# Kernel tuning notes

Hardware: AMD Instinct MI355X
Metric: run time of the kernel (lower is better)

Reference implementation:

```python
import jax, jax.numpy as jnp
import numpy as np

B, N, C = 1, 384, 64
H = 1  # num_heads

def setup_inputs() -> dict:
    key = jax.random.key(0)
    k1, k2 = jax.random.split(key)
    x = jax.random.normal(k1, (B, N, C), dtype=jnp.float32)
    # Linear(dim, 8*dim, bias=False) weight, torch layout [out, in]; scaled for sane logits
    w_w = jax.random.normal(k2, (8 * C, C), dtype=jnp.float32) * 0.05
    return {"x": x, "w_w": w_w}

def reference(x, w_w):
    Bx, Nx, Cx = x.shape
    D = Cx // H
    scale = D ** (-0.5)
    # [B,N,8C] -> [8,B,H,N,D]
    w = (x @ w_w.T).reshape(Bx, Nx, 8, H, D).transpose(2, 0, 3, 1, 4)
    a, b, c, d, e, f, v1, v2 = (w[i] for i in range(8))
    AB = jnp.einsum('bhid,bhjd->bhij', a, b) * scale  # scores over (i,j)
    CD = jnp.einsum('bhid,bhkd->bhik', c, d) * scale  # scores over (i,k)
    EF = jnp.einsum('bhjd,bhkd->bhjk', e, f) * scale  # scores over (j,k)
    # A_IJK[b,h,i,j,k] = AB[i,j] + CD[i,k] + EF[j,k]
    A = AB[:, :, :, :, None] + CD[:, :, :, None, :] + EF[:, :, None, :, :]
    # original subtracts the GLOBAL max of the whole tensor
    eA = jnp.exp(A - jnp.max(A))
    # V[b,h,j,k,d] = v1[j,d] * v2[k,d]
    V = v1[:, :, :, None, :] * v2[:, :, None, :, :]
    num = jnp.einsum('bhijk,bhjkd->bhid', eA, V)  # sum over j,k (avoids N^3*D blowup)
    den = jnp.sum(eA, axis=(-2, -1))[..., None]   # [B,H,N,1]
    out = num / den
    # [B,H,N,D] -> [B,N,C]  (forward returns before self.proj)
    return jnp.transpose(out, (0, 2, 1, 3)).reshape(Bx, Nx, Cx)
```

## Files before the change

kernel.cpp:

```cpp
#include <hip/hip_runtime.h>
#include <math.h>


#define NN 384

using short8 = __attribute__((ext_vector_type(8))) short;
using f32x4  = __attribute__((ext_vector_type(4))) float;
typedef unsigned short u16;
typedef unsigned int u32;

__global__ void proj_kernel(const float* __restrict__ x, const float* __restrict__ W,
                            float* __restrict__ proj, float* __restrict__ v1t,
                            float* __restrict__ v2t) {
    int n = blockIdx.x;
    __shared__ float xs[64];
    if (threadIdx.x < 64) xs[threadIdx.x] = x[n * 64 + threadIdx.x];
    __syncthreads();
    const float4* xv4 = (const float4*)xs;
    for (int r = 0; r < 2; ++r) {
        int o = threadIdx.x + r * 256;
        const float4* w4 = (const float4*)(W + o * 64);
        float s = 0.f;
#pragma unroll
        for (int c = 0; c < 16; ++c) {
            float4 wv = w4[c];
            float4 xv = xv4[c];
            s += wv.x * xv.x + wv.y * xv.y + wv.z * xv.z + wv.w * xv.w;
        }
        proj[n * 512 + o] = s;
        if (o >= 448)      v2t[(o - 448) * NN + n] = s;
        else if (o >= 384) v1t[(o - 384) * NN + n] = s;
    }
}

__global__ void scores_exp_kernel(const float* __restrict__ proj,
                                  float* __restrict__ R, float* __restrict__ P,
                                  u16* __restrict__ Qhi, u16* __restrict__ Qlo) {
    int m = blockIdx.z;
    int bi = blockIdx.y, bj = blockIdx.x;
    int tid = threadIdx.x;
    int tx = tid % 16, ty = tid / 16;
    int aoff, boff;
    if (m == 0)      { aoff = 0;   boff = 64;  }
    else if (m == 1) { aoff = 128; boff = 192; }
    else             { aoff = 256; boff = 320; }

    __shared__ float As[32][65], Bs[32][65];
    for (int r = 0; r < 8; ++r) {
        int idx = tid + r * 256;
        int row = idx / 64, col = idx % 64;
        As[row][col] = proj[(bi * 32 + row) * 512 + aoff + col];
        Bs[row][col] = proj[(bj * 32 + row) * 512 + boff + col];
    }
    __syncthreads();

    float acc[2][2] = {{0.f, 0.f}, {0.f, 0.f}};
#pragma unroll 8
    for (int d = 0; d < 64; ++d) {
        float a0 = As[ty * 2][d], a1 = As[ty * 2 + 1][d];
        float b0 = Bs[tx * 2][d], b1 = Bs[tx * 2 + 1][d];
        acc[0][0] += a0 * b0; acc[0][1] += a0 * b1;
        acc[1][0] += a1 * b0; acc[1][1] += a1 * b1;
    }
#pragma unroll
    for (int a = 0; a < 2; ++a) {
        int row = bi * 32 + ty * 2 + a;
        int col = bj * 32 + tx * 2;
        float v0 = expf(acc[a][0] * 0.125f);
        float v1 = expf(acc[a][1] * 0.125f);
        if (m == 0) {
            R[row * NN + col] = v0; R[row * NN + col + 1] = v1;
        } else if (m == 1) {
            P[row * NN + col] = v0; P[row * NN + col + 1] = v1;
        } else {
            u32 b0 = __float_as_uint(v0), b1 = __float_as_uint(v1);
            u32 h0 = b0 & 0xFFFF0000u,   h1 = b1 & 0xFFFF0000u;
            float l0 = v0 - __uint_as_float(h0);
            float l1 = v1 - __uint_as_float(h1);
            ushort2 hw, lw;
            hw.x = (u16)(h0 >> 16); hw.y = (u16)(h1 >> 16);
            lw.x = (u16)(__float_as_uint(l0) >> 16);
            lw.y = (u16)(__float_as_uint(l1) >> 16);
            *(ushort2*)(Qhi + row * NN + col) = hw;
            *(ushort2*)(Qlo + row * NN + col) = lw;
        }
    }
}

#define MFMA(A, B, C) __builtin_amdgcn_mfma_f32_16x16x32_bf16(A, B, C, 0, 0, 0)

__global__ __launch_bounds__(256, 3) void main_mfma(
    const u16* __restrict__ Qhi, const u16* __restrict__ Qlo,
    const float* __restrict__ R, const float* __restrict__ P,
    const float* __restrict__ v1t, const float* __restrict__ v2t,
    float* __restrict__ num0, float* __restrict__ num1,
    float* __restrict__ den0, float* __restrict__ den1) {
    int i  = blockIdx.x >> 1;
    int jh = blockIdx.x & 1;
    int tid = (int)threadIdx.x;
    int w = tid >> 6, l = tid & 63;
    int lr = l & 15, lc = l >> 4;
    int j0 = jh * 192 + w * 48;

    __shared__ float p_s[NN];
    __shared__ u16 Bh[2][80 * 40];
    __shared__ u16 Bl[2][80 * 40];
    __shared__ float sh[4][80];

    p_s[tid] = P[i * NN + tid];
    if (tid < 128) p_s[256 + tid] = P[i * NN + 256 + tid];

    f32x4 acc[3][5];
#pragma unroll
    for (int mf = 0; mf < 3; ++mf)
#pragma unroll
        for (int nf = 0; nf < 5; ++nf)
            acc[mf][nf] = (f32x4){0.f, 0.f, 0.f, 0.f};

    __syncthreads();

    auto BUILD = [&](int buf, int k0) {
        {
            int n = tid >> 2, kk = (tid & 3) * 8;
            const float* vp = v2t + n * NN + k0 + kk;
            float4 va = *(const float4*)vp;
            float4 vb = *(const float4*)(vp + 4);
            float pr[8] = {va.x * p_s[k0 + kk + 0], va.y * p_s[k0 + kk + 1],
                           va.z * p_s[k0 + kk + 2], va.w * p_s[k0 + kk + 3],
                           vb.x * p_s[k0 + kk + 4], vb.y * p_s[k0 + kk + 5],
                           vb.z * p_s[k0 + kk + 6], vb.w * p_s[k0 + kk + 7]};
            u32* dh = (u32*)&Bh[buf][n * 40 + kk];
            u32* dl = (u32*)&Bl[buf][n * 40 + kk];
#pragma unroll
            for (int e = 0; e < 4; ++e) {
                float x0 = pr[2 * e], x1 = pr[2 * e + 1];
                u32 h0 = __float_as_uint(x0) & 0xFFFF0000u;
                u32 h1 = __float_as_uint(x1) & 0xFFFF0000u;
                float l0 = x0 - __uint_as_float(h0);
                float l1 = x1 - __uint_as_float(h1);
                dh[e] = (h0 >> 16) | h1;
                dl[e] = (__float_as_uint(l0) >> 16) |
                        (__float_as_uint(l1) & 0xFFFF0000u);
            }
        }
        if (tid < 64) {
            int n = 64 + (tid >> 2), kk = (tid & 3) * 8;
            u32* dh = (u32*)&Bh[buf][n * 40 + kk];
            u32* dl = (u32*)&Bl[buf][n * 40 + kk];
            if (n == 64) {
#pragma unroll
                for (int e = 0; e < 4; ++e) {
                    float x0 = p_s[k0 + kk + 2 * e], x1 = p_s[k0 + kk + 2 * e + 1];
                    u32 h0 = __float_as_uint(x0) & 0xFFFF0000u;
                    u32 h1 = __float_as_uint(x1) & 0xFFFF0000u;
                    float l0 = x0 - __uint_as_float(h0);
                    float l1 = x1 - __uint_as_float(h1);
                    dh[e] = (h0 >> 16) | h1;
                    dl[e] = (__float_as_uint(l0) >> 16) |
                            (__float_as_uint(l1) & 0xFFFF0000u);
                }
            } else {
#pragma unroll
                for (int e = 0; e < 4; ++e) { dh[e] = 0u; dl[e] = 0u; }
            }
        }
    };

    BUILD(0, 0);
    __syncthreads();

    for (int t = 0; t < 12; ++t) {
        int b = t & 1;
        int k8 = t * 32 + lc * 8;
        short8 ahi[3], alo[3];
#pragma unroll
        for (int mf = 0; mf < 3; ++mf) {
            int j = j0 + mf * 16 + lr;
            ahi[mf] = *(const short8*)(Qhi + j * NN + k8);
            alo[mf] = *(const short8*)(Qlo + j * NN + k8);
        }
        if (t < 11) BUILD(b ^ 1, (t + 1) * 32);
#pragma unroll
        for (int nf = 0; nf < 5; ++nf) {
            short8 bh = *(const short8*)&Bh[b][(nf * 16 + lr) * 40 + lc * 8];
            short8 bl = *(const short8*)&Bl[b][(nf * 16 + lr) * 40 + lc * 8];
#pragma unroll
            for (int mf = 0; mf < 3; ++mf) {
                acc[mf][nf] = MFMA(ahi[mf], bh, acc[mf][nf]);
                acc[mf][nf] = MFMA(ahi[mf], bl, acc[mf][nf]);
                acc[mf][nf] = MFMA(alo[mf], bh, acc[mf][nf]);
            }
        }
        __syncthreads();
    }

    float4 rj[3];
#pragma unroll
    for (int mf = 0; mf < 3; ++mf)
        rj[mf] = *(const float4*)(R + i * NN + j0 + mf * 16 + lc * 4);

#pragma unroll
    for (int nf = 0; nf < 5; ++nf) {
        float s = 0.f;
#pragma unroll
        for (int mf = 0; mf < 3; ++mf) {
            f32x4 a = acc[mf][nf];
            if (nf < 4) {
                const float* vp = v1t + (nf * 16 + lr) * NN + j0 + mf * 16 + lc * 4;
                float4 v1v = *(const float4*)vp;
                s += a[0] * rj[mf].x * v1v.x + a[1] * rj[mf].y * v1v.y
                   + a[2] * rj[mf].z * v1v.z + a[3] * rj[mf].w * v1v.w;
            } else {
                s += a[0] * rj[mf].x + a[1] * rj[mf].y
                   + a[2] * rj[mf].z + a[3] * rj[mf].w;
            }
        }
        s += __shfl_xor(s, 16, 64);
        s += __shfl_xor(s, 32, 64);
        if (l < 16) sh[w][nf * 16 + l] = s;
    }
    __syncthreads();
    if (tid < 80) {
        float v = sh[0][tid] + sh[1][tid] + sh[2][tid] + sh[3][tid];
        if (tid < 64) (jh ? num1 : num0)[i * 64 + tid] = v;
        else if (tid == 64) (jh ? den1 : den0)[i] = v;
    }
}

__global__ void finalize_kernel(const float* __restrict__ num0, const float* __restrict__ num1,
                                const float* __restrict__ den0, const float* __restrict__ den1,
                                float* __restrict__ out) {
    int idx = blockIdx.x * 256 + threadIdx.x;
    int i = idx >> 6;
    out[idx] = (num0[idx] + num1[idx]) / (den0[i] + den1[i]);
}

extern "C" void kernel_launch(void* const* d_in, const int* in_sizes, int n_in,
                              void* d_out, int out_size, void* d_ws, size_t ws_size,
                              hipStream_t stream) {
    const float* x = (const float*)d_in[0];
    const float* W = (const float*)d_in[1];
    float* out = (float*)d_out;

    float* ws   = (float*)d_ws;
    float* R    = ws;
    float* P    = ws + 147456;
    float* v1t  = ws + 294912;
    float* v2t  = ws + 319488;
    u16*   Qhi  = (u16*)(ws + 344064);
    u16*   Qlo  = (u16*)(ws + 417792);
    float* proj = ws + 491520;
    float* num0 = proj;
    float* num1 = proj + 24576;
    float* den0 = proj + 49152;
    float* den1 = proj + 49536;

    proj_kernel<<<NN, 256, 0, stream>>>(x, W, proj, v1t, v2t);
    scores_exp_kernel<<<dim3(12, 12, 3), 256, 0, stream>>>(proj, R, P, Qhi, Qlo);
    main_mfma<<<768, 256, 0, stream>>>(Qhi, Qlo, R, P, v1t, v2t,
                                       num0, num1, den0, den1);
    finalize_kernel<<<96, 256, 0, stream>>>(num0, num1, den0, den1, out);
}
```

Measured before the change: 105.9 us.

## Split k reduction across two blocks and reduce four partials in finalize

The main MFMA kernel now splits the k dimension in half, so 1536 blocks each run 6 k-steps instead of 768 blocks running 12. Each block writes its partial numerator and denominator to one of four slots, and the finalize kernel sums them. Zero-padding rows are cleared once at kernel start instead of inside every build step, the k loop is fully unrolled, and the launch-bounds occupancy hint rises from 3 to 4. This aims to fill more CUs and shorten the serial k loop, at the cost of extra partial writes and more register pressure from the higher occupancy target.

```diff
diff --git a/kernel.cpp b/kernel.cpp
--- a/kernel.cpp
+++ b/kernel.cpp
@@ -89,26 +89,32 @@
 
 #define MFMA(A, B, C) __builtin_amdgcn_mfma_f32_16x16x32_bf16(A, B, C, 0, 0, 0)
 
-__global__ __launch_bounds__(256, 3) void main_mfma(
+__global__ __launch_bounds__(256, 4) void main_mfma(
     const u16* __restrict__ Qhi, const u16* __restrict__ Qlo,
     const float* __restrict__ R, const float* __restrict__ P,
     const float* __restrict__ v1t, const float* __restrict__ v2t,
-    float* __restrict__ num0, float* __restrict__ num1,
-    float* __restrict__ den0, float* __restrict__ den1) {
-    int i  = blockIdx.x >> 1;
-    int jh = blockIdx.x & 1;
+    float* __restrict__ numP, float* __restrict__ denP) {
+    int bid = blockIdx.x;
+    int i  = bid >> 2;
+    int jh = (bid >> 1) & 1;
+    int kh = bid & 1;
     int tid = (int)threadIdx.x;
     int w = tid >> 6, l = tid & 63;
     int lr = l & 15, lc = l >> 4;
     int j0 = jh * 192 + w * 48;
-
-    __shared__ float p_s[NN];
+    int kbase = kh * 192;
+
+    __shared__ float p_s[192];
     __shared__ u16 Bh[2][80 * 40];
     __shared__ u16 Bl[2][80 * 40];
     __shared__ float sh[4][80];
 
-    p_s[tid] = P[i * NN + tid];
-    if (tid < 128) p_s[256 + tid] = P[i * NN + 256 + tid];
+    if (tid < 192) p_s[tid] = P[i * NN + kbase + tid];
+    for (int z = tid; z < 1200; z += 256) {
+        int m = z / 300, r = z % 300;
+        u32* base = (u32*)((m & 1) ? Bl[m >> 1] : Bh[m >> 1]);
+        base[1300 + r] = 0u;
+    }
 
     f32x4 acc[3][5];
 #pragma unroll
@@ -119,16 +125,16 @@
 
     __syncthreads();
 
-    auto BUILD = [&](int buf, int k0) {
+    auto BUILD = [&](int buf, int t) {
+        int krel = t * 32;
         {
             int n = tid >> 2, kk = (tid & 3) * 8;
-            const float* vp = v2t + n * NN + k0 + kk;
+            const float* vp = v2t + n * NN + kbase + krel + kk;
             float4 va = *(const float4*)vp;
             float4 vb = *(const float4*)(vp + 4);
-            float pr[8] = {va.x * p_s[k0 + kk + 0], va.y * p_s[k0 + kk + 1],
-                           va.z * p_s[k0 + kk + 2], va.w * p_s[k0 + kk + 3],
-                           vb.x * p_s[k0 + kk + 4], vb.y * p_s[k0 + kk + 5],
-                           vb.z * p_s[k0 + kk + 6], vb.w * p_s[k0 + kk + 7]};
+            const float* pp = p_s + krel + kk;
+            float pr[8] = {va.x * pp[0], va.y * pp[1], va.z * pp[2], va.w * pp[3],
+                           vb.x * pp[4], vb.y * pp[5], vb.z * pp[6], vb.w * pp[7]};
             u32* dh = (u32*)&Bh[buf][n * 40 + kk];
             u32* dl = (u32*)&Bl[buf][n * 40 + kk];
 #pragma unroll
@@ -143,25 +149,21 @@
                         (__float_as_uint(l1) & 0xFFFF0000u);
             }
         }
-        if (tid < 64) {
-            int n = 64 + (tid >> 2), kk = (tid & 3) * 8;
-            u32* dh = (u32*)&Bh[buf][n * 40 + kk];
-            u32* dl = (u32*)&Bl[buf][n * 40 + kk];
-            if (n == 64) {
-#pragma unroll
-                for (int e = 0; e < 4; ++e) {
-                    float x0 = p_s[k0 + kk + 2 * e], x1 = p_s[k0 + kk + 2 * e + 1];
-                    u32 h0 = __float_as_uint(x0) & 0xFFFF0000u;
-                    u32 h1 = __float_as_uint(x1) & 0xFFFF0000u;
-                    float l0 = x0 - __uint_as_float(h0);
-                    float l1 = x1 - __uint_as_float(h1);
-                    dh[e] = (h0 >> 16) | h1;
-                    dl[e] = (__float_as_uint(l0) >> 16) |
-                            (__float_as_uint(l1) & 0xFFFF0000u);
-                }
-            } else {
-#pragma unroll
-                for (int e = 0; e < 4; ++e) { dh[e] = 0u; dl[e] = 0u; }
+        if (tid < 4) {
+            int kk = tid * 8;
+            const float* pp = p_s + krel + kk;
+            u32* dh = (u32*)&Bh[buf][64 * 40 + kk];
+            u32* dl = (u32*)&Bl[buf][64 * 40 + kk];
+#pragma unroll
+            for (int e = 0; e < 4; ++e) {
+                float x0 = pp[2 * e], x1 = pp[2 * e + 1];
+                u32 h0 = __float_as_uint(x0) & 0xFFFF0000u;
+                u32 h1 = __float_as_uint(x1) & 0xFFFF0000u;
+                float l0 = x0 - __uint_as_float(h0);
+                float l1 = x1 - __uint_as_float(h1);
+                dh[e] = (h0 >> 16) | h1;
+                dl[e] = (__float_as_uint(l0) >> 16) |
+                        (__float_as_uint(l1) & 0xFFFF0000u);
             }
         }
     };
@@ -169,9 +171,10 @@
     BUILD(0, 0);
     __syncthreads();
 
-    for (int t = 0; t < 12; ++t) {
+#pragma unroll
+    for (int t = 0; t < 6; ++t) {
         int b = t & 1;
-        int k8 = t * 32 + lc * 8;
+        int k8 = kbase + t * 32 + lc * 8;
         short8 ahi[3], alo[3];
 #pragma unroll
         for (int mf = 0; mf < 3; ++mf) {
@@ -179,7 +182,7 @@
             ahi[mf] = *(const short8*)(Qhi + j * NN + k8);
             alo[mf] = *(const short8*)(Qlo + j * NN + k8);
         }
-        if (t < 11) BUILD(b ^ 1, (t + 1) * 32);
+        if (t < 5) BUILD(b ^ 1, t + 1);
 #pragma unroll
         for (int nf = 0; nf < 5; ++nf) {
             short8 bh = *(const short8*)&Bh[b][(nf * 16 + lr) * 40 + lc * 8];
@@ -222,17 +225,20 @@
     __syncthreads();
     if (tid < 80) {
         float v = sh[0][tid] + sh[1][tid] + sh[2][tid] + sh[3][tid];
-        if (tid < 64) (jh ? num1 : num0)[i * 64 + tid] = v;
-        else if (tid == 64) (jh ? den1 : den0)[i] = v;
-    }
-}
-
-__global__ void finalize_kernel(const float* __restrict__ num0, const float* __restrict__ num1,
-                                const float* __restrict__ den0, const float* __restrict__ den1,
+        int q = jh * 2 + kh;
+        if (tid < 64)       numP[q * 24576 + i * 64 + tid] = v;
+        else if (tid == 64) denP[q * 384 + i] = v;
+    }
+}
+
+__global__ void finalize_kernel(const float* __restrict__ numP,
+                                const float* __restrict__ denP,
                                 float* __restrict__ out) {
     int idx = blockIdx.x * 256 + threadIdx.x;
     int i = idx >> 6;
-    out[idx] = (num0[idx] + num1[idx]) / (den0[i] + den1[i]);
+    float n = numP[idx] + numP[24576 + idx] + numP[49152 + idx] + numP[73728 + idx];
+    float d = denP[i] + denP[384 + i] + denP[768 + i] + denP[1152 + i];
+    out[idx] = n / d;
 }
 
 extern "C" void kernel_launch(void* const* d_in, const int* in_sizes, int n_in,
@@ -250,14 +256,11 @@
     u16*   Qhi  = (u16*)(ws + 344064);
     u16*   Qlo  = (u16*)(ws + 417792);
     float* proj = ws + 491520;
-    float* num0 = proj;
-    float* num1 = proj + 24576;
-    float* den0 = proj + 49152;
-    float* den1 = proj + 49536;
+    float* numP = proj;
+    float* denP = proj + 98304;
 
     proj_kernel<<<NN, 256, 0, stream>>>(x, W, proj, v1t, v2t);
     scores_exp_kernel<<<dim3(12, 12, 3), 256, 0, stream>>>(proj, R, P, Qhi, Qlo);
-    main_mfma<<<768, 256, 0, stream>>>(Qhi, Qlo, R, P, v1t, v2t,
-                                       num0, num1, den0, den1);
-    finalize_kernel<<<96, 256, 0, stream>>>(num0, num1, den0, den1, out);
-}
+    main_mfma<<<1536, 256, 0, stream>>>(Qhi, Qlo, R, P, v1t, v2t, numP, denP);
+    finalize_kernel<<<96, 256, 0, stream>>>(numP, denP, out);
+}
```

After: 124.0 us. 1.17x slower.

## Software-pipeline A and V loads with double-buffered registers and pre-zeroed padding rows

Applied to the files above, without the earlier changes.

Restructures the main MFMA loop so global loads of the Q hi/lo A-fragments and the v2t values are issued one or two tiles ahead into double-buffered registers. The loop is unrolled by two with fixed LDS buffers. The zero padding rows of the B tiles are now cleared once at kernel start instead of on every build, and only 4 threads write the P row. The goal is to hide global memory latency behind the MFMAs and to cut redundant LDS writes, at the cost of more registers, which could lower occupancy under launch_bounds(256,3).

```diff
diff --git a/kernel.cpp b/kernel.cpp
--- a/kernel.cpp
+++ b/kernel.cpp
@@ -101,6 +101,8 @@
     int w = tid >> 6, l = tid & 63;
     int lr = l & 15, lc = l >> 4;
     int j0 = jh * 192 + w * 48;
+    int kkq = (tid & 3) * 8;
+    int nB  = tid >> 2;
 
     __shared__ float p_s[NN];
     __shared__ u16 Bh[2][80 * 40];
@@ -109,6 +111,15 @@
 
     p_s[tid] = P[i * NN + tid];
     if (tid < 128) p_s[256 + tid] = P[i * NN + 256 + tid];
+    for (int z = tid; z < 1200; z += 256) {
+        int m = z / 300, r = z % 300;
+        u32* base = (u32*)((m & 1) ? Bl[m >> 1] : Bh[m >> 1]);
+        base[1300 + r] = 0u;
+    }
+
+    const u16* qh_base = Qhi + (j0 + lr) * NN + lc * 8;
+    const u16* ql_base = Qlo + (j0 + lr) * NN + lc * 8;
+    const float* vt_base = v2t + nB * NN + kkq;
 
     f32x4 acc[3][5];
 #pragma unroll
@@ -117,80 +128,88 @@
         for (int nf = 0; nf < 5; ++nf)
             acc[mf][nf] = (f32x4){0.f, 0.f, 0.f, 0.f};
 
-    __syncthreads();
-
-    auto BUILD = [&](int buf, int k0) {
-        {
-            int n = tid >> 2, kk = (tid & 3) * 8;
-            const float* vp = v2t + n * NN + k0 + kk;
-            float4 va = *(const float4*)vp;
-            float4 vb = *(const float4*)(vp + 4);
-            float pr[8] = {va.x * p_s[k0 + kk + 0], va.y * p_s[k0 + kk + 1],
-                           va.z * p_s[k0 + kk + 2], va.w * p_s[k0 + kk + 3],
-                           vb.x * p_s[k0 + kk + 4], vb.y * p_s[k0 + kk + 5],
-                           vb.z * p_s[k0 + kk + 6], vb.w * p_s[k0 + kk + 7]};
-            u32* dh = (u32*)&Bh[buf][n * 40 + kk];
-            u32* dl = (u32*)&Bl[buf][n * 40 + kk];
+    auto LOADA = [&](short8* H, short8* L, int t) {
+#pragma unroll
+        for (int mf = 0; mf < 3; ++mf) {
+            H[mf] = *(const short8*)(qh_base + mf * 16 * NN + t * 32);
+            L[mf] = *(const short8*)(ql_base + mf * 16 * NN + t * 32);
+        }
+    };
+    auto LOADV = [&](float4& a, float4& b, int t) {
+        a = *(const float4*)(vt_base + t * 32);
+        b = *(const float4*)(vt_base + t * 32 + 4);
+    };
+    auto BUILDW = [&](int buf, float4 va, float4 vb, int t) {
+        int krel = t * 32;
+        const float* pp = p_s + krel + kkq;
+        float pr[8] = {va.x * pp[0], va.y * pp[1], va.z * pp[2], va.w * pp[3],
+                       vb.x * pp[4], vb.y * pp[5], vb.z * pp[6], vb.w * pp[7]};
+        u32* dh = (u32*)&Bh[buf][nB * 40 + kkq];
+        u32* dl = (u32*)&Bl[buf][nB * 40 + kkq];
+#pragma unroll
+        for (int e = 0; e < 4; ++e) {
+            float x0 = pr[2 * e], x1 = pr[2 * e + 1];
+            u32 h0 = __float_as_uint(x0) & 0xFFFF0000u;
+            u32 h1 = __float_as_uint(x1) & 0xFFFF0000u;
+            float l0 = x0 - __uint_as_float(h0);
+            float l1 = x1 - __uint_as_float(h1);
+            dh[e] = (h0 >> 16) | h1;
+            dl[e] = (__float_as_uint(l0) >> 16) |
+                    (__float_as_uint(l1) & 0xFFFF0000u);
+        }
+        if (tid < 4) {
+            const float* pq = p_s + krel + tid * 8;
+            u32* eh = (u32*)&Bh[buf][64 * 40 + tid * 8];
+            u32* el = (u32*)&Bl[buf][64 * 40 + tid * 8];
 #pragma unroll
             for (int e = 0; e < 4; ++e) {
-                float x0 = pr[2 * e], x1 = pr[2 * e + 1];
+                float x0 = pq[2 * e], x1 = pq[2 * e + 1];
                 u32 h0 = __float_as_uint(x0) & 0xFFFF0000u;
                 u32 h1 = __float_as_uint(x1) & 0xFFFF0000u;
                 float l0 = x0 - __uint_as_float(h0);
                 float l1 = x1 - __uint_as_float(h1);
-                dh[e] = (h0 >> 16) | h1;
-                dl[e] = (__float_as_uint(l0) >> 16) |
+                eh[e] = (h0 >> 16) | h1;
+                el[e] = (__float_as_uint(l0) >> 16) |
                         (__float_as_uint(l1) & 0xFFFF0000u);
             }
         }
-        if (tid < 64) {
-            int n = 64 + (tid >> 2), kk = (tid & 3) * 8;
-            u32* dh = (u32*)&Bh[buf][n * 40 + kk];
-            u32* dl = (u32*)&Bl[buf][n * 40 + kk];
-            if (n == 64) {
-#pragma unroll
-                for (int e = 0; e < 4; ++e) {
-                    float x0 = p_s[k0 + kk + 2 * e], x1 = p_s[k0 + kk + 2 * e + 1];
-                    u32 h0 = __float_as_uint(x0) & 0xFFFF0000u;
-                    u32 h1 = __float_as_uint(x1) & 0xFFFF0000u;
-                    float l0 = x0 - __uint_as_float(h0);
-                    float l1 = x1 - __uint_as_float(h1);
-                    dh[e] = (h0 >> 16) | h1;
-                    dl[e] = (__float_as_uint(l0) >> 16) |
-                            (__float_as_uint(l1) & 0xFFFF0000u);
-                }
-            } else {
-#pragma unroll
-                for (int e = 0; e < 4; ++e) { dh[e] = 0u; dl[e] = 0u; }
-            }
-        }
-    };
-
-    BUILD(0, 0);
-    __syncthreads();
-
-    for (int t = 0; t < 12; ++t) {
-        int b = t & 1;
-        int k8 = t * 32 + lc * 8;
-        short8 ahi[3], alo[3];
-#pragma unroll
-        for (int mf = 0; mf < 3; ++mf) {
-            int j = j0 + mf * 16 + lr;
-            ahi[mf] = *(const short8*)(Qhi + j * NN + k8);
-            alo[mf] = *(const short8*)(Qlo + j * NN + k8);
-        }
-        if (t < 11) BUILD(b ^ 1, (t + 1) * 32);
+    };
+    auto MFMASTEP = [&](int b, short8* aH, short8* aL) {
 #pragma unroll
         for (int nf = 0; nf < 5; ++nf) {
             short8 bh = *(const short8*)&Bh[b][(nf * 16 + lr) * 40 + lc * 8];
             short8 bl = *(const short8*)&Bl[b][(nf * 16 + lr) * 40 + lc * 8];
 #pragma unroll
             for (int mf = 0; mf < 3; ++mf) {
-                acc[mf][nf] = MFMA(ahi[mf], bh, acc[mf][nf]);
-                acc[mf][nf] = MFMA(ahi[mf], bl, acc[mf][nf]);
-                acc[mf][nf] = MFMA(alo[mf], bh, acc[mf][nf]);
+                acc[mf][nf] = MFMA(aH[mf], bh, acc[mf][nf]);
+                acc[mf][nf] = MFMA(aH[mf], bl, acc[mf][nf]);
+                acc[mf][nf] = MFMA(aL[mf], bh, acc[mf][nf]);
             }
         }
+    };
+
+    short8 aH0[3], aL0[3], aH1[3], aL1[3];
+    float4 vA0, vB0, vA1, vB1;
+
+    LOADA(aH0, aL0, 0); LOADA(aH1, aL1, 1);
+    LOADV(vA0, vB0, 0); LOADV(vA1, vB1, 1);
+    __syncthreads();
+    BUILDW(0, vA0, vB0, 0);
+    LOADV(vA0, vB0, 2);
+    __syncthreads();
+
+#pragma unroll
+    for (int tt = 0; tt < 6; ++tt) {
+        int t0 = tt * 2, t1 = tt * 2 + 1;
+        BUILDW(1, vA1, vB1, t0 + 1);
+        if (t0 + 3 <= 11) LOADV(vA1, vB1, t0 + 3);
+        MFMASTEP(0, aH0, aL0);
+        if (t0 + 2 <= 11) LOADA(aH0, aL0, t0 + 2);
+        __syncthreads();
+        if (t1 < 11) BUILDW(0, vA0, vB0, t1 + 1);
+        if (t1 + 3 <= 11) LOADV(vA0, vB0, t1 + 3);
+        MFMASTEP(1, aH1, aL1);
+        if (t1 + 2 <= 11) LOADA(aH1, aL1, t1 + 2);
         __syncthreads();
     }
 
```

Result: slower. 108.6 us (+2.6%).
